# Kernel optimization log

Hardware: AMD Instinct MI355X
Metric: run time of the kernel (lower is better)

The kernel has to match this reference:

```python
import jax, jax.numpy as jnp
import numpy as np

N_NODES, N_EDGES, F_IN = 8192, 32768, 16
N_SUB, N_GRAPH = 512, 32
EDGE_DIM, HID = 5, 128
DIMS = [(16, 32), (32, 64), (64, 64)]  # (M_in, M_out) per NNConv layer


def _segment_mean(x, seg, n):
    s = jax.ops.segment_sum(x, seg, num_segments=n)
    c = jax.ops.segment_sum(jnp.ones((x.shape[0], 1), x.dtype), seg, num_segments=n)
    return s / jnp.maximum(c, 1.0)


def _nnconv(x, src, dst, eattr, W1, b1, W2, b2, root, bias):
    # edge MLP -> per-edge weight matrix theta: [E, M_in, M_out]
    h = jax.nn.relu(eattr @ W1 + b1)
    theta = (h @ W2 + b2).reshape(-1, x.shape[1], root.shape[1])
    msg = jnp.einsum('ei,eio->eo', x[src], theta)          # gather + per-edge matvec
    agg = jax.ops.segment_sum(msg, dst, num_segments=x.shape[0])  # scatter-add (aggr='add')
    return agg + x @ root + bias


def setup_inputs() -> dict:
    key = jax.random.key(0)
    ks = jax.random.split(key, 32)
    inp = {}
    inp['x'] = jax.random.normal(ks[0], (N_NODES, F_IN), jnp.float32)
    inp['edge_index'] = jax.random.randint(ks[1], (2, N_EDGES), 0, N_NODES)
    inp['edge_attr'] = jax.random.uniform(ks[2], (N_EDGES, EDGE_DIM), jnp.float32)
    inp['node_to_subgraph'] = jnp.sort(jax.random.randint(ks[3], (N_NODES,), 0, N_SUB))
    inp['subgraph_to_graph'] = jnp.sort(jax.random.randint(ks[4], (N_SUB,), 0, N_GRAPH))
    i = 5
    for l, (ci, co) in enumerate(DIMS):
        inp[f'W1_{l}'] = jax.random.normal(ks[i], (EDGE_DIM, HID), jnp.float32) * 0.1
        inp[f'b1_{l}'] = jnp.zeros((HID,), jnp.float32)
        inp[f'W2_{l}'] = jax.random.normal(ks[i + 1], (HID, ci * co), jnp.float32) * 0.05
        inp[f'b2_{l}'] = jnp.zeros((ci * co,), jnp.float32)
        inp[f'root_{l}'] = jax.random.normal(ks[i + 2], (ci, co), jnp.float32) * 0.1
        inp[f'bias_{l}'] = jnp.zeros((co,), jnp.float32)
        i += 3
    inp['fc1_w'] = jax.random.normal(ks[i], (64, 32), jnp.float32) * 0.1
    inp['fc1_b'] = jnp.zeros((32,), jnp.float32)
    inp['fc2_w'] = jax.random.normal(ks[i + 1], (32, 16), jnp.float32) * 0.1
    inp['fc2_b'] = jnp.zeros((16,), jnp.float32)
    inp['fc3_w'] = jax.random.normal(ks[i + 2], (16, 1), jnp.float32) * 0.1
    inp['fc3_b'] = jnp.zeros((1,), jnp.float32)
    return inp


def reference(x, edge_index, edge_attr, node_to_subgraph, subgraph_to_graph,
              W1_0, b1_0, W2_0, b2_0, root_0, bias_0,
              W1_1, b1_1, W2_1, b2_1, root_1, bias_1,
              W1_2, b1_2, W2_2, b2_2, root_2, bias_2,
              fc1_w, fc1_b, fc2_w, fc2_b, fc3_w, fc3_b):
    src, dst = edge_index[0], edge_index[1]
    layers = [(W1_0, b1_0, W2_0, b2_0, root_0, bias_0),
              (W1_1, b1_1, W2_1, b2_1, root_1, bias_1),
              (W1_2, b1_2, W2_2, b2_2, root_2, bias_2)]
    h = x
    for (W1, b1, W2, b2, root, bias) in layers:
        h = jax.nn.elu(_nnconv(h, src, dst, edge_attr, W1, b1, W2, b2, root, bias))
    h = _segment_mean(h, node_to_subgraph, N_SUB)      # global_mean_pool over subgraphs
    h = _segment_mean(h, subgraph_to_graph, N_GRAPH)   # global_mean_pool over graphs
    h = jax.nn.elu(h @ fc1_w + fc1_b)
    h = jax.nn.elu(h @ fc2_w + fc2_b)
    return (h @ fc3_w + fc3_b).reshape(-1)
```

## Files before the change

kernel.cpp:

```cpp
#include <hip/hip_runtime.h>

#define E_EDGES 32768
#define NN 8192
#define HID 128
#define KS 4

typedef _Float16 half8 __attribute__((ext_vector_type(8)));
typedef _Float16 half4 __attribute__((ext_vector_type(4)));
typedef float f32x4 __attribute__((ext_vector_type(4)));

__global__ void hist_k(const int* __restrict__ dst, int* __restrict__ hist) {
  int e = blockIdx.x * 256 + threadIdx.x;
  if (e < E_EDGES) atomicAdd(&hist[dst[e]], 1);
}

__global__ void scan_k(const int* __restrict__ hist, int* __restrict__ roff, int* __restrict__ cursor) {
  __shared__ int wsum[16];
  int t = threadIdx.x;
  int lane = t & 63, wv = t >> 6;
  int base = t * 8;
  int loc[8]; int s = 0;
#pragma unroll
  for (int j = 0; j < 8; ++j) { loc[j] = s; s += hist[base + j]; }
  int inc = s;
#pragma unroll
  for (int off = 1; off < 64; off <<= 1) {
    int u = __shfl_up(inc, off, 64);
    if (lane >= off) inc += u;
  }
  if (lane == 63) wsum[wv] = inc;
  __syncthreads();
  if (t < 64) {
    int u = (t < 16) ? wsum[t] : 0;
#pragma unroll
    for (int off = 1; off < 16; off <<= 1) {
      int x = __shfl_up(u, off, 64);
      if (lane >= off) u += x;
    }
    if (t < 16) wsum[t] = u;
  }
  __syncthreads();
  int excl = (wv ? wsum[wv - 1] : 0) + inc - s;
#pragma unroll
  for (int j = 0; j < 8; ++j) { int v = excl + loc[j]; roff[base + j] = v; cursor[base + j] = v; }
  if (t == 1023) roff[NN] = wsum[15];
}

__global__ void scatter_k(const int* __restrict__ dst, int* __restrict__ cursor, int* __restrict__ eidx) {
  int e = blockIdx.x * 256 + threadIdx.x;
  if (e < E_EDGES) { int p = atomicAdd(&cursor[dst[e]], 1); eidx[p] = e; }
}

template <int CI, int CO>
__device__ inline void prep8(int h8, const float* __restrict__ W2,
                             const float* __restrict__ b2, _Float16* __restrict__ out) {
  constexpr int Kmain = 128 * CI;
  constexpr int FC = CO / 16;
  int lane = h8 & 63;
  int quad = lane >> 4, l15 = lane & 15;
  int rest = h8 >> 6;
  int fc = rest & (FC - 1);
  int c = rest / FC;
  int k0 = c * 32 + quad * 8;
  int n = fc * 16 + l15;
  half8 r;
#pragma unroll
  for (int j = 0; j < 8; ++j) {
    int k = k0 + j;
    float v = 0.f;
    if (k < Kmain) v = W2[(size_t)k * CO + n];
    else if (k < Kmain + CI) v = b2[(k - Kmain) * CO + n];
    r[j] = (_Float16)v;
  }
  *(half8*)(out + (size_t)h8 * 8) = r;
}

__global__ void prep_zero_k(const float* __restrict__ W2_0, const float* __restrict__ b2_0, _Float16* __restrict__ o0,
                            const float* __restrict__ W2_1, const float* __restrict__ b2_1, _Float16* __restrict__ o1,
                            const float* __restrict__ W2_2, const float* __restrict__ b2_2, _Float16* __restrict__ o2,
                            int4* __restrict__ hist4, float4* __restrict__ pools4) {
  constexpr int H0 = 2176 * 32 / 8;
  constexpr int H1 = 4224 * 64 / 8;
  constexpr int H2 = 8320 * 64 / 8;
  constexpr int HT = H0 + H1 + H2;
  constexpr int ZH = NN / 4;
  constexpr int ZP = (512 * 64 + 512) / 4;
  int tid = blockIdx.x * 256 + threadIdx.x;
  if (tid < H0) prep8<16, 32>(tid, W2_0, b2_0, o0);
  else if (tid < H0 + H1) prep8<32, 64>(tid - H0, W2_1, b2_1, o1);
  else if (tid < HT) prep8<64, 64>(tid - H0 - H1, W2_2, b2_2, o2);
  else if (tid < HT + ZH) hist4[tid - HT] = int4{0, 0, 0, 0};
  else if (tid < HT + ZH + ZP) pools4[tid - HT - ZH] = float4{0.f, 0.f, 0.f, 0.f};
}

__device__ inline half8 pack8(float4 a, float4 b) {
  half8 r;
  r[0] = (_Float16)a.x; r[1] = (_Float16)a.y; r[2] = (_Float16)a.z; r[3] = (_Float16)a.w;
  r[4] = (_Float16)b.x; r[5] = (_Float16)b.y; r[6] = (_Float16)b.z; r[7] = (_Float16)b.w;
  return r;
}

__device__ __forceinline__ void gload_lds16(const _Float16* g, _Float16* l) {
  __builtin_amdgcn_global_load_lds(
      (__attribute__((address_space(1))) void*)(size_t)(const void*)g,
      (__attribute__((address_space(3))) void*)(size_t)(void*)l, 16, 0, 0);
}

template <int CI, int CO>
__launch_bounds__(256, 2)
__global__ void msg_mfma_k(const float* __restrict__ xcur, const int* __restrict__ src,
                           const float* __restrict__ eattr, const float* __restrict__ W1,
                           const float* __restrict__ b1, const _Float16* __restrict__ Bsw,
                           float* __restrict__ msgbuf) {
  constexpr int ME = 256;
  constexpr int HSTR = 36;
  constexpr int FC = CO / 16;
  constexpr int FCW = FC / 2;
  constexpr int FR = 8;
  constexpr int NMAIN = CI / 4;
  constexpr int XPN = (CI == 64) ? 2 : 1;
  constexpr int RHALF = 4 * FC * 64 * 8;

  __shared__ _Float16 he_s[ME * HSTR];
  __shared__ float ea_s[ME * 5];
  __shared__ float W1s[5 * 32];
  __shared__ float b1s[32];
  __shared__ int src_s[ME];
  __shared__ _Float16 bls[2 * RHALF];

  int t = threadIdx.x;
  int e0 = blockIdx.x * ME;
  int y = blockIdx.y;
  int hbeg = y * 32;

  for (int j = t; j < ME * 5; j += 256) ea_s[j] = eattr[e0 * 5 + j];
  if (t < 5 * 32) W1s[t] = W1[(t >> 5) * HID + hbeg + (t & 31)];
  if (t < 32) b1s[t] = b1[hbeg + t];
  src_s[t] = src[e0 + t];
  __syncthreads();

  for (int j = t; j < 32 * ME; j += 256) {
    int hl = j & 31, e = j >> 5;
    float v = b1s[hl];
#pragma unroll
    for (int d = 0; d < 5; ++d) v += ea_s[e * 5 + d] * W1s[d * 32 + hl];
    he_s[e * HSTR + hl] = (_Float16)fmaxf(v, 0.f);
  }
  __syncthreads();

  int lane = t & 63;
  int w = t >> 6;
  int we = w & 1, wn = w >> 1;
  int quad = lane >> 4, l15 = lane & 15;
  int qsh = (quad >> 1) << 4;
  int Rg0 = y * NMAIN;
  int NR = NMAIN + ((y == 3) ? 1 : 0);

  half8 xp[FR][XPN];
  int hoff[FR];
#pragma unroll
  for (int fr = 0; fr < FR; ++fr) {
    int e = we * 128 + fr * 16 + l15;
    const float* xr = xcur + (size_t)src_s[e] * CI;
    int i0 = (CI == 16) ? ((quad & 1) * 8) : (quad * 8);
    float4 v0 = *(const float4*)(xr + i0);
    float4 v1 = *(const float4*)(xr + i0 + 4);
    xp[fr][0] = pack8(v0, v1);
    if constexpr (CI == 64) {
      float4 v2 = *(const float4*)(xr + i0 + 32);
      float4 v3 = *(const float4*)(xr + i0 + 36);
      xp[fr][1] = pack8(v2, v3);
    }
    hoff[fr] = e * HSTR;
  }

  f32x4 acc[FR][FCW];
#pragma unroll
  for (int fr = 0; fr < FR; ++fr)
#pragma unroll
    for (int fc = 0; fc < FCW; ++fc)
#pragma unroll
      for (int r = 0; r < 4; ++r) acc[fr][fc][r] = 0.f;

  auto stageR = [&](int rg, int buf) {
    const _Float16* gb = Bsw + (size_t)rg * RHALF + w * (FC * 512);
    _Float16* lb = bls + buf * RHALF + w * (FC * 512);
#pragma unroll
    for (int i = 0; i < FC; ++i)
      gload_lds16(gb + i * 512 + lane * 8, lb + i * 512);
  };

  stageR(Rg0, 0);
  stageR(Rg0 + 1, 1);

  for (int r = 0; r < NR; ++r) {
    if (r + 1 < NR) {
      if constexpr (FC == 4) asm volatile("s_waitcnt vmcnt(4)" ::: "memory");
      else                   asm volatile("s_waitcnt vmcnt(2)" ::: "memory");
    } else {
      asm volatile("s_waitcnt vmcnt(0)" ::: "memory");
    }
    __builtin_amdgcn_s_barrier();

    const _Float16* bp = bls + (r & 1) * RHALF;
    int c0 = (Rg0 + r) * 4;

    if (r < NMAIN) {
      unsigned int hp2[FR];
      half4 hp4[FR];
      if constexpr (CI == 64) {
        int oh = (c0 >> 1) - hbeg;
#pragma unroll
        for (int fr = 0; fr < FR; ++fr) hp2[fr] = *(const unsigned int*)(he_s + hoff[fr] + oh);
      } else if constexpr (CI == 32) {
        int oh = c0 - hbeg;
#pragma unroll
        for (int fr = 0; fr < FR; ++fr) hp4[fr] = *(const half4*)(he_s + hoff[fr] + oh);
      }
#pragma unroll
      for (int cr = 0; cr < 4; ++cr) {
        int c = c0 + cr;
        half8 a[FR];
#pragma unroll
        for (int fr = 0; fr < FR; ++fr) {
          if constexpr (CI == 64) {
            unsigned short hb = (unsigned short)((cr >= 2) ? (hp2[fr] >> 16) : hp2[fr]);
            _Float16 hv = __builtin_bit_cast(_Float16, hb);
            a[fr] = xp[fr][cr & 1] * hv;
          } else if constexpr (CI == 32) {
            a[fr] = xp[fr][0] * hp4[fr][cr];
          } else {
            unsigned int hw = *(const unsigned int*)(he_s + hoff[fr] + (2 * c - hbeg));
            _Float16 hv = __builtin_bit_cast(_Float16, (unsigned short)(hw >> qsh));
            a[fr] = xp[fr][0] * hv;
          }
        }
#pragma unroll
        for (int fc = 0; fc < FCW; ++fc) {
          half8 bf = *(const half8*)&bp[((cr * FC + wn * FCW + fc) * 64 + lane) * 8];
#pragma unroll
          for (int fr = 0; fr < FR; ++fr)
            acc[fr][fc] = __builtin_amdgcn_mfma_f32_16x16x32_f16(a[fr], bf, acc[fr][fc], 0, 0, 0);
        }
      }
    } else {
#pragma unroll
      for (int cr = 0; cr < 4; ++cr) {
        half8 a[FR];
#pragma unroll
        for (int fr = 0; fr < FR; ++fr) a[fr] = xp[fr][(CI == 64) ? (cr & 1) : 0];
#pragma unroll
        for (int fc = 0; fc < FCW; ++fc) {
          half8 bf = *(const half8*)&bp[((cr * FC + wn * FCW + fc) * 64 + lane) * 8];
#pragma unroll
          for (int fr = 0; fr < FR; ++fr)
            acc[fr][fc] = __builtin_amdgcn_mfma_f32_16x16x32_f16(a[fr], bf, acc[fr][fc], 0, 0, 0);
        }
      }
    }

    asm volatile("s_waitcnt lgkmcnt(0)" ::: "memory");
    __builtin_amdgcn_s_barrier();
    if (r + 2 < NR) stageR(Rg0 + r + 2, r & 1);
  }

  float* mb = msgbuf + ((size_t)y * E_EDGES + e0) * CO;
#pragma unroll
  for (int fr = 0; fr < FR; ++fr)
#pragma unroll
    for (int fc = 0; fc < FCW; ++fc)
#pragma unroll
      for (int r = 0; r < 4; ++r) {
        int el = we * 128 + fr * 16 + quad * 4 + r;
        int o = (wn * FCW + fc) * 16 + l15;
        mb[el * CO + o] = acc[fr][fc][r];
      }
}

template <int CI, int CO, bool POOL>
__global__ void gather_elu_k(const float* __restrict__ xcur, const float* __restrict__ root,
                             const float* __restrict__ bias, const float* __restrict__ msgbuf,
                             const int* __restrict__ roff, const int* __restrict__ eidx,
                             float* __restrict__ xnext, const int* __restrict__ n2s,
                             float* __restrict__ ssum, float* __restrict__ scnt) {
  constexpr int OV = CO / 4;
  constexpr int NB = 256 / OV;
  __shared__ float xs[NB * CI];
  int t = threadIdx.x;
  int n0 = blockIdx.x * NB;
  for (int j = t; j < NB * CI; j += 256) xs[j] = xcur[n0 * CI + j];
  __syncthreads();
  int nl = t / OV, o4 = t & (OV - 1);
  int n = n0 + nl;
  float4 a = ((const float4*)bias)[o4];
  const float4* root4 = (const float4*)root;
#pragma unroll
  for (int i = 0; i < CI; ++i) {
    float xv = xs[nl * CI + i];
    float4 rv = root4[i * OV + o4];
    a.x += xv * rv.x; a.y += xv * rv.y; a.z += xv * rv.z; a.w += xv * rv.w;
  }
  int j1 = roff[n + 1];
  const float4* mb4 = (const float4*)msgbuf;
  for (int j = roff[n]; j < j1; ++j) {
    int e = eidx[j];
#pragma unroll
    for (int s = 0; s < KS; ++s) {
      float4 m = mb4[((size_t)s * E_EDGES + e) * OV + o4];
      a.x += m.x; a.y += m.y; a.z += m.z; a.w += m.w;
    }
  }
  float4 v;
  v.x = a.x > 0.f ? a.x : expm1f(a.x);
  v.y = a.y > 0.f ? a.y : expm1f(a.y);
  v.z = a.z > 0.f ? a.z : expm1f(a.z);
  v.w = a.w > 0.f ? a.w : expm1f(a.w);
  if constexpr (POOL) {
    int s = n2s[n];
    float* sb = &ssum[(s << 6) + o4 * 4];
    atomicAdd(sb + 0, v.x); atomicAdd(sb + 1, v.y);
    atomicAdd(sb + 2, v.z); atomicAdd(sb + 3, v.w);
    if (o4 == 0) atomicAdd(&scnt[s], 1.f);
  } else {
    ((float4*)xnext)[(size_t)n * OV + o4] = v;
  }
}

__global__ void pg_head_k(const float* __restrict__ ssum, const float* __restrict__ scnt,
                          const int* __restrict__ s2g,
                          const float* __restrict__ w1, const float* __restrict__ b1,
                          const float* __restrict__ w2, const float* __restrict__ b2,
                          const float* __restrict__ w3, const float* __restrict__ b3,
                          float* __restrict__ out) {
  int g = blockIdx.x;
  int t = threadIdx.x;
  __shared__ int s2s[512];
  __shared__ float hm[64], h1[32], h2[16];
  for (int i = t; i < 512; i += 64) s2s[i] = s2g[i];
  __syncthreads();
  float acc = 0.f, cnt = 0.f;
  for (int s = 0; s < 512; ++s) {
    if (s2s[s] == g) {
      acc += ssum[(s << 6) + t] / fmaxf(scnt[s], 1.f);
      cnt += 1.f;
    }
  }
  hm[t] = acc / fmaxf(cnt, 1.f);
  __syncthreads();
  if (t < 32) {
    float a = b1[t];
    for (int i = 0; i < 64; ++i) a += hm[i] * w1[i * 32 + t];
    h1[t] = a > 0.f ? a : expm1f(a);
  }
  __syncthreads();
  if (t < 16) {
    float a = b2[t];
    for (int i = 0; i < 32; ++i) a += h1[i] * w2[i * 16 + t];
    h2[t] = a > 0.f ? a : expm1f(a);
  }
  __syncthreads();
  if (t == 0) {
    float a = b3[0];
    for (int i = 0; i < 16; ++i) a += h2[i] * w3[i];
    out[g] = a;
  }
}

extern "C" void kernel_launch(void* const* d_in, const int* in_sizes, int n_in,
                              void* d_out, int out_size, void* d_ws, size_t ws_size,
                              hipStream_t stream) {
  (void)in_sizes; (void)n_in; (void)out_size; (void)ws_size;
  const float* x0 = (const float*)d_in[0];
  const int* ei = (const int*)d_in[1];
  const float* ea = (const float*)d_in[2];
  const int* n2s = (const int*)d_in[3];
  const int* s2g = (const int*)d_in[4];
  const float* W1_[3] = {(const float*)d_in[5], (const float*)d_in[11], (const float*)d_in[17]};
  const float* b1_[3] = {(const float*)d_in[6], (const float*)d_in[12], (const float*)d_in[18]};
  const float* W2_[3] = {(const float*)d_in[7], (const float*)d_in[13], (const float*)d_in[19]};
  const float* b2_[3] = {(const float*)d_in[8], (const float*)d_in[14], (const float*)d_in[20]};
  const float* rt_[3] = {(const float*)d_in[9], (const float*)d_in[15], (const float*)d_in[21]};
  const float* bs_[3] = {(const float*)d_in[10], (const float*)d_in[16], (const float*)d_in[22]};
  const float* fc1w = (const float*)d_in[23]; const float* fc1b = (const float*)d_in[24];
  const float* fc2w = (const float*)d_in[25]; const float* fc2b = (const float*)d_in[26];
  const float* fc3w = (const float*)d_in[27]; const float* fc3b = (const float*)d_in[28];
  float* out = (float*)d_out;

  const int* srcp = ei;
  const int* dstp = ei + E_EDGES;

  char* wsb = (char*)d_ws;
  size_t off = 0;
  auto alloc = [&](size_t bytes) {
    void* p = wsb + off;
    off += (bytes + 255) & ~(size_t)255;
    return p;
  };
  _Float16* Bsw0 = (_Float16*)alloc((size_t)2176 * 32 * 2);
  _Float16* Bsw1 = (_Float16*)alloc((size_t)4224 * 64 * 2);
  _Float16* Bsw2 = (_Float16*)alloc((size_t)8320 * 64 * 2);
  float* msgbuf = (float*)alloc((size_t)KS * E_EDGES * 64 * 4);
  float* x1 = (float*)alloc((size_t)NN * 32 * 4);
  float* x2 = (float*)alloc((size_t)NN * 64 * 4);
  int* hist = (int*)alloc((size_t)NN * 4);
  int* roff = (int*)alloc((size_t)(NN + 1) * 4);
  int* cursor = (int*)alloc((size_t)NN * 4);
  int* eidx = (int*)alloc((size_t)E_EDGES * 4);
  const int npool = 512 * 64 + 512;
  float* pools = (float*)alloc((size_t)npool * 4);
  float* ssum = pools;
  float* scnt = pools + 512 * 64;

  const int nprep = 109056 + 2048 + 8320;
  prep_zero_k<<<(nprep + 255) / 256, 256, 0, stream>>>(
      W2_[0], b2_[0], Bsw0, W2_[1], b2_[1], Bsw1, W2_[2], b2_[2], Bsw2,
      (int4*)hist, (float4*)pools);
  hist_k<<<E_EDGES / 256, 256, 0, stream>>>(dstp, hist);
  scan_k<<<1, 1024, 0, stream>>>(hist, roff, cursor);
  scatter_k<<<E_EDGES / 256, 256, 0, stream>>>(dstp, cursor, eidx);

  dim3 mg(E_EDGES / 256, KS);
  msg_mfma_k<16, 32><<<mg, 256, 0, stream>>>(x0, srcp, ea, W1_[0], b1_[0], Bsw0, msgbuf);
  gather_elu_k<16, 32, false><<<NN / 32, 256, 0, stream>>>(x0, rt_[0], bs_[0], msgbuf, roff, eidx, x1, nullptr, nullptr, nullptr);
  msg_mfma_k<32, 64><<<mg, 256, 0, stream>>>(x1, srcp, ea, W1_[1], b1_[1], Bsw1, msgbuf);
  gather_elu_k<32, 64, false><<<NN / 16, 256, 0, stream>>>(x1, rt_[1], bs_[1], msgbuf, roff, eidx, x2, nullptr, nullptr, nullptr);
  msg_mfma_k<64, 64><<<mg, 256, 0, stream>>>(x2, srcp, ea, W1_[2], b1_[2], Bsw2, msgbuf);
  gather_elu_k<64, 64, true><<<NN / 16, 256, 0, stream>>>(x2, rt_[2], bs_[2], msgbuf, roff, eidx, nullptr, n2s, ssum, scnt);

  pg_head_k<<<32, 64, 0, stream>>>(ssum, scnt, s2g, fc1w, fc1b, fc2w, fc2b, fc3w, fc3b, out);
}
```

Before: 287.1 us.

## Process edges in dst-sorted order and store messages edge-major for contiguous gather

The message kernel now walks edges in CSR (destination-sorted) order through eidx, gathering src and edge attributes indirectly. It writes each edge's per-slice partial messages contiguously as [edge][slice][CO], so the gather kernel reads one contiguous run per destination node and no longer needs the eidx indirection. It also reassigns warps so each warp covers 64 edges across all output columns instead of 128 edges across half of them, which changes register use and per-warp LDS B-fragment reads. The cost is extra indirect loads of src and eattr in the message kernel.

Result: faster. 278.6 us (median of 2 runs) (-3.0%).

```diff
diff --git a/kernel.cpp b/kernel.cpp
--- a/kernel.cpp
+++ b/kernel.cpp
@@ -109,14 +109,13 @@
 template <int CI, int CO>
 __launch_bounds__(256, 2)
 __global__ void msg_mfma_k(const float* __restrict__ xcur, const int* __restrict__ src,
+                           const int* __restrict__ eidx,
                            const float* __restrict__ eattr, const float* __restrict__ W1,
                            const float* __restrict__ b1, const _Float16* __restrict__ Bsw,
                            float* __restrict__ msgbuf) {
   constexpr int ME = 256;
   constexpr int HSTR = 36;
   constexpr int FC = CO / 16;
-  constexpr int FCW = FC / 2;
-  constexpr int FR = 8;
   constexpr int NMAIN = CI / 4;
   constexpr int XPN = (CI == 64) ? 2 : 1;
   constexpr int RHALF = 4 * FC * 64 * 8;
@@ -133,10 +132,14 @@
   int y = blockIdx.y;
   int hbeg = y * 32;
 
-  for (int j = t; j < ME * 5; j += 256) ea_s[j] = eattr[e0 * 5 + j];
+  {
+    int eg = eidx[e0 + t];
+    src_s[t] = src[eg];
+#pragma unroll
+    for (int d = 0; d < 5; ++d) ea_s[t * 5 + d] = eattr[eg * 5 + d];
+  }
   if (t < 5 * 32) W1s[t] = W1[(t >> 5) * HID + hbeg + (t & 31)];
   if (t < 32) b1s[t] = b1[hbeg + t];
-  src_s[t] = src[e0 + t];
   __syncthreads();
 
   for (int j = t; j < 32 * ME; j += 256) {
@@ -150,17 +153,16 @@
 
   int lane = t & 63;
   int w = t >> 6;
-  int we = w & 1, wn = w >> 1;
   int quad = lane >> 4, l15 = lane & 15;
   int qsh = (quad >> 1) << 4;
   int Rg0 = y * NMAIN;
   int NR = NMAIN + ((y == 3) ? 1 : 0);
 
-  half8 xp[FR][XPN];
-  int hoff[FR];
-#pragma unroll
-  for (int fr = 0; fr < FR; ++fr) {
-    int e = we * 128 + fr * 16 + l15;
+  half8 xp[4][XPN];
+  int hoff[4];
+#pragma unroll
+  for (int fr = 0; fr < 4; ++fr) {
+    int e = w * 64 + fr * 16 + l15;
     const float* xr = xcur + (size_t)src_s[e] * CI;
     int i0 = (CI == 16) ? ((quad & 1) * 8) : (quad * 8);
     float4 v0 = *(const float4*)(xr + i0);
@@ -174,11 +176,11 @@
     hoff[fr] = e * HSTR;
   }
 
-  f32x4 acc[FR][FCW];
-#pragma unroll
-  for (int fr = 0; fr < FR; ++fr)
-#pragma unroll
-    for (int fc = 0; fc < FCW; ++fc)
+  f32x4 acc[4][FC];
+#pragma unroll
+  for (int fr = 0; fr < 4; ++fr)
+#pragma unroll
+    for (int fc = 0; fc < FC; ++fc)
 #pragma unroll
       for (int r = 0; r < 4; ++r) acc[fr][fc][r] = 0.f;
 
@@ -206,23 +208,23 @@
     int c0 = (Rg0 + r) * 4;
 
     if (r < NMAIN) {
-      unsigned int hp2[FR];
-      half4 hp4[FR];
+      unsigned int hp2[4];
+      half4 hp4[4];
       if constexpr (CI == 64) {
         int oh = (c0 >> 1) - hbeg;
 #pragma unroll
-        for (int fr = 0; fr < FR; ++fr) hp2[fr] = *(const unsigned int*)(he_s + hoff[fr] + oh);
+        for (int fr = 0; fr < 4; ++fr) hp2[fr] = *(const unsigned int*)(he_s + hoff[fr] + oh);
       } else if constexpr (CI == 32) {
         int oh = c0 - hbeg;
 #pragma unroll
-        for (int fr = 0; fr < FR; ++fr) hp4[fr] = *(const half4*)(he_s + hoff[fr] + oh);
+        for (int fr = 0; fr < 4; ++fr) hp4[fr] = *(const half4*)(he_s + hoff[fr] + oh);
       }
 #pragma unroll
       for (int cr = 0; cr < 4; ++cr) {
         int c = c0 + cr;
-        half8 a[FR];
-#pragma unroll
-        for (int fr = 0; fr < FR; ++fr) {
+        half8 a[4];
+#pragma unroll
+        for (int fr = 0; fr < 4; ++fr) {
           if constexpr (CI == 64) {
             unsigned short hb = (unsigned short)((cr >= 2) ? (hp2[fr] >> 16) : hp2[fr]);
             _Float16 hv = __builtin_bit_cast(_Float16, hb);
@@ -236,24 +238,24 @@
           }
         }
 #pragma unroll
-        for (int fc = 0; fc < FCW; ++fc) {
-          half8 bf = *(const half8*)&bp[((cr * FC + wn * FCW + fc) * 64 + lane) * 8];
-#pragma unroll
-          for (int fr = 0; fr < FR; ++fr)
+        for (int fc = 0; fc < FC; ++fc) {
+          half8 bf = *(const half8*)&bp[((cr * FC + fc) * 64 + lane) * 8];
+#pragma unroll
+          for (int fr = 0; fr < 4; ++fr)
             acc[fr][fc] = __builtin_amdgcn_mfma_f32_16x16x32_f16(a[fr], bf, acc[fr][fc], 0, 0, 0);
         }
       }
     } else {
 #pragma unroll
       for (int cr = 0; cr < 4; ++cr) {
-        half8 a[FR];
-#pragma unroll
-        for (int fr = 0; fr < FR; ++fr) a[fr] = xp[fr][(CI == 64) ? (cr & 1) : 0];
-#pragma unroll
-        for (int fc = 0; fc < FCW; ++fc) {
-          half8 bf = *(const half8*)&bp[((cr * FC + wn * FCW + fc) * 64 + lane) * 8];
-#pragma unroll
-          for (int fr = 0; fr < FR; ++fr)
+        half8 a[4];
+#pragma unroll
+        for (int fr = 0; fr < 4; ++fr) a[fr] = xp[fr][(CI == 64) ? (cr & 1) : 0];
+#pragma unroll
+        for (int fc = 0; fc < FC; ++fc) {
+          half8 bf = *(const half8*)&bp[((cr * FC + fc) * 64 + lane) * 8];
+#pragma unroll
+          for (int fr = 0; fr < 4; ++fr)
             acc[fr][fc] = __builtin_amdgcn_mfma_f32_16x16x32_f16(a[fr], bf, acc[fr][fc], 0, 0, 0);
         }
       }
@@ -264,23 +266,22 @@
     if (r + 2 < NR) stageR(Rg0 + r + 2, r & 1);
   }
 
-  float* mb = msgbuf + ((size_t)y * E_EDGES + e0) * CO;
-#pragma unroll
-  for (int fr = 0; fr < FR; ++fr)
-#pragma unroll
-    for (int fc = 0; fc < FCW; ++fc)
+#pragma unroll
+  for (int fr = 0; fr < 4; ++fr)
+#pragma unroll
+    for (int fc = 0; fc < FC; ++fc)
 #pragma unroll
       for (int r = 0; r < 4; ++r) {
-        int el = we * 128 + fr * 16 + quad * 4 + r;
-        int o = (wn * FCW + fc) * 16 + l15;
-        mb[el * CO + o] = acc[fr][fc][r];
+        int el = w * 64 + fr * 16 + quad * 4 + r;
+        int o = fc * 16 + l15;
+        msgbuf[((size_t)(e0 + el) * KS + y) * CO + o] = acc[fr][fc][r];
       }
 }
 
 template <int CI, int CO, bool POOL>
 __global__ void gather_elu_k(const float* __restrict__ xcur, const float* __restrict__ root,
                              const float* __restrict__ bias, const float* __restrict__ msgbuf,
-                             const int* __restrict__ roff, const int* __restrict__ eidx,
+                             const int* __restrict__ roff,
                              float* __restrict__ xnext, const int* __restrict__ n2s,
                              float* __restrict__ ssum, float* __restrict__ scnt) {
   constexpr int OV = CO / 4;
@@ -302,11 +303,10 @@
   }
   int j1 = roff[n + 1];
   const float4* mb4 = (const float4*)msgbuf;
-  for (int j = roff[n]; j < j1; ++j) {
-    int e = eidx[j];
+  for (int p = roff[n]; p < j1; ++p) {
 #pragma unroll
     for (int s = 0; s < KS; ++s) {
-      float4 m = mb4[((size_t)s * E_EDGES + e) * OV + o4];
+      float4 m = mb4[((size_t)p * KS + s) * OV + o4];
       a.x += m.x; a.y += m.y; a.z += m.z; a.w += m.w;
     }
   }
@@ -420,12 +420,12 @@
   scatter_k<<<E_EDGES / 256, 256, 0, stream>>>(dstp, cursor, eidx);
 
   dim3 mg(E_EDGES / 256, KS);
-  msg_mfma_k<16, 32><<<mg, 256, 0, stream>>>(x0, srcp, ea, W1_[0], b1_[0], Bsw0, msgbuf);
-  gather_elu_k<16, 32, false><<<NN / 32, 256, 0, stream>>>(x0, rt_[0], bs_[0], msgbuf, roff, eidx, x1, nullptr, nullptr, nullptr);
-  msg_mfma_k<32, 64><<<mg, 256, 0, stream>>>(x1, srcp, ea, W1_[1], b1_[1], Bsw1, msgbuf);
-  gather_elu_k<32, 64, false><<<NN / 16, 256, 0, stream>>>(x1, rt_[1], bs_[1], msgbuf, roff, eidx, x2, nullptr, nullptr, nullptr);
-  msg_mfma_k<64, 64><<<mg, 256, 0, stream>>>(x2, srcp, ea, W1_[2], b1_[2], Bsw2, msgbuf);
-  gather_elu_k<64, 64, true><<<NN / 16, 256, 0, stream>>>(x2, rt_[2], bs_[2], msgbuf, roff, eidx, nullptr, n2s, ssum, scnt);
+  msg_mfma_k<16, 32><<<mg, 256, 0, stream>>>(x0, srcp, eidx, ea, W1_[0], b1_[0], Bsw0, msgbuf);
+  gather_elu_k<16, 32, false><<<NN / 32, 256, 0, stream>>>(x0, rt_[0], bs_[0], msgbuf, roff, x1, nullptr, nullptr, nullptr);
+  msg_mfma_k<32, 64><<<mg, 256, 0, stream>>>(x1, srcp, eidx, ea, W1_[1], b1_[1], Bsw1, msgbuf);
+  gather_elu_k<32, 64, false><<<NN / 16, 256, 0, stream>>>(x1, rt_[1], bs_[1], msgbuf, roff, x2, nullptr, nullptr, nullptr);
+  msg_mfma_k<64, 64><<<mg, 256, 0, stream>>>(x2, srcp, eidx, ea, W1_[2], b1_[2], Bsw2, msgbuf);
+  gather_elu_k<64, 64, true><<<NN / 16, 256, 0, stream>>>(x2, rt_[2], bs_[2], msgbuf, roff, nullptr, n2s, ssum, scnt);
 
   pg_head_k<<<32, 64, 0, stream>>>(ssum, scnt, s2g, fc1w, fc1b, fc2w, fc2b, fc3w, fc3b, out);
 }
```
